# Kernel optimization log

Measured on AMD Instinct MI355X. Metric: run time of the kernel, lower is better.

The kernel has to match this reference:

```python
import jax, jax.numpy as jnp
import numpy as np

NUM_CHANS = 64
LAG = 5
HIDDEN = [32, 32]  # module appends a final 1-channel layer
BATCH = 16
T = 2048


def setup_inputs() -> dict:
    key = jax.random.key(0)
    ks = jax.random.split(key, 7)
    p, h0, h1 = NUM_CHANS, HIDDEN[0], HIDDEN[1]
    # Per-network weights stacked along leading axis n = num_series = p.
    # Xavier-ish scale for layer 0 (Conv1d(p, h0, lag)), default-ish for rest.
    s0 = float(np.sqrt(2.0 / (p * LAG + h0)))
    return {
        "X": jax.random.normal(ks[0], (BATCH, T, p), dtype=jnp.float32),
        "W0": jax.random.normal(ks[1], (p, h0, p, LAG), dtype=jnp.float32) * s0,
        "b0": jax.random.normal(ks[2], (p, h0), dtype=jnp.float32) * 0.01,
        "W1": jax.random.normal(ks[3], (p, h1, h0), dtype=jnp.float32) * float(np.sqrt(1.0 / h0)),
        "b1": jax.random.normal(ks[4], (p, h1), dtype=jnp.float32) * 0.01,
        "W2": jax.random.normal(ks[5], (p, 1, h1), dtype=jnp.float32) * float(np.sqrt(1.0 / h1)),
        "b2": jax.random.normal(ks[6], (p, 1), dtype=jnp.float32) * 0.01,
    }


def reference(X, W0, b0, W1, b1, W2, b2):
    # X: [B, T, p]. Each of n=p networks: Conv1d(p,h0,lag) -> ReLU -> Conv1d(h0,h1,1)
    # -> ReLU -> Conv1d(h1,1,1); outputs concatenated along last dim.
    lag = W0.shape[-1]
    Tout = X.shape[1] - lag + 1  # valid conv output length
    # Sliding windows: Xwin[b,t,c,l] = X[b, t+l, c]  -> [B, Tout, p, lag]
    Xwin = jnp.stack([X[:, l:l + Tout, :] for l in range(lag)], axis=-1)
    # Layer 0 across all n networks at once: [B, n, Tout, h0]
    h = jnp.einsum('btcl,nhcl->bnth', Xwin, W0) + b0[None, :, None, :]
    # 1x1 conv layers (per-network dense along channel dim)
    h = jax.nn.relu(h)
    h = jnp.einsum('bnti,noi->bnto', h, W1) + b1[None, :, None, :]
    h = jax.nn.relu(h)
    h = jnp.einsum('bnti,noi->bnto', h, W2) + b2[None, :, None, :]  # [B, n, Tout, 1]
    # concat along dim 2 of (batch, Tout, 1) per network -> (B, Tout, n)
    return jnp.transpose(h[..., 0], (0, 2, 1))
```

## Files before the change

kernel.cpp:

```cpp
#include <hip/hip_runtime.h>

#define NCH 64
#define LAG 5
#define H0 32
#define H1 32
#define TIN 2048
#define TOUT 2044
#define NBATCH 16

#define XSTRIDE 72

typedef __attribute__((ext_vector_type(8))) short short8;
typedef __attribute__((ext_vector_type(4))) short short4v;
typedef __attribute__((ext_vector_type(4))) float f32x4;

__device__ __forceinline__ unsigned short f2bf(float f) {
    unsigned u = __float_as_uint(f);
    u += 0x7fffu + ((u >> 16) & 1u);
    return (unsigned short)(u >> 16);
}

__device__ __forceinline__ unsigned pack2bf_relu(float a, float b) {
    unsigned ua = __float_as_uint(fmaxf(a, 0.0f)) + 0x8000u;
    unsigned ub = __float_as_uint(fmaxf(b, 0.0f)) + 0x8000u;
    return __builtin_amdgcn_perm(ub, ua, 0x07060302u);
}

__device__ __forceinline__ short4v pack4bf_relu(const f32x4& v) {
    union { short4v s; unsigned u[2]; } cv;
    cv.u[0] = pack2bf_relu(v[0], v[1]);
    cv.u[1] = pack2bf_relu(v[2], v[3]);
    return cv.s;
}

__global__ __launch_bounds__(256) void prep_all(
    const float* __restrict__ X,  unsigned short* __restrict__ Xpad,
    const float* __restrict__ W0, unsigned short* __restrict__ W0b,
    const float* __restrict__ W1, unsigned short* __restrict__ W1b,
    const float* __restrict__ W2, unsigned short* __restrict__ W2b)
{
    const int bx = blockIdx.x;
    if (bx < 512) {
        int id  = bx * 256 + threadIdx.x;
        int row = id >> 2, s4 = id & 3;
        const float4* src = (const float4*)(X + (size_t)id * 16);
        unsigned long long v[4];
        #pragma unroll
        for (int k = 0; k < 4; ++k) {
            float4 x = src[k];
            v[k] = (unsigned long long)f2bf(x.x)
                 | ((unsigned long long)f2bf(x.y) << 16)
                 | ((unsigned long long)f2bf(x.z) << 32)
                 | ((unsigned long long)f2bf(x.w) << 48);
        }
        unsigned long long* dst = (unsigned long long*)(Xpad + (size_t)row * XSTRIDE + s4 * 16);
        dst[0] = v[0]; dst[1] = v[1]; dst[2] = v[2]; dst[3] = v[3];
    } else if (bx < 1024) {
        int j = (bx - 512) * 256 + threadIdx.x;
        int nh = j >> 6, c = j & 63;
        const float* src = W0 + (size_t)j * LAG;
        unsigned short* dst = W0b + nh * 320 + c;
        #pragma unroll
        for (int l = 0; l < LAG; ++l) dst[l * 64] = f2bf(src[l]);
    } else if (bx < 1056) {
        int i = ((bx - 1024) * 256 + threadIdx.x) * 8;
        float4 a = *(const float4*)(W1 + i);
        float4 b = *(const float4*)(W1 + i + 4);
        unsigned long long v0 = (unsigned long long)f2bf(a.x)
                              | ((unsigned long long)f2bf(a.y) << 16)
                              | ((unsigned long long)f2bf(a.z) << 32)
                              | ((unsigned long long)f2bf(a.w) << 48);
        unsigned long long v1 = (unsigned long long)f2bf(b.x)
                              | ((unsigned long long)f2bf(b.y) << 16)
                              | ((unsigned long long)f2bf(b.z) << 32)
                              | ((unsigned long long)f2bf(b.w) << 48);
        *(unsigned long long*)(W1b + i)     = v0;
        *(unsigned long long*)(W1b + i + 4) = v1;
    } else {
        int i = threadIdx.x * 8;
        float4 a = *(const float4*)(W2 + i);
        float4 b = *(const float4*)(W2 + i + 4);
        unsigned long long v0 = (unsigned long long)f2bf(a.x)
                              | ((unsigned long long)f2bf(a.y) << 16)
                              | ((unsigned long long)f2bf(a.z) << 32)
                              | ((unsigned long long)f2bf(a.w) << 48);
        unsigned long long v1 = (unsigned long long)f2bf(b.x)
                              | ((unsigned long long)f2bf(b.y) << 16)
                              | ((unsigned long long)f2bf(b.z) << 32)
                              | ((unsigned long long)f2bf(b.w) << 48);
        *(unsigned long long*)(W2b + i)     = v0;
        *(unsigned long long*)(W2b + i + 4) = v1;
    }
}

__global__ __launch_bounds__(256, 3) void mlp_mfma(
    const unsigned short* __restrict__ Xpad,
    const unsigned short* __restrict__ W0b,
    const unsigned short* __restrict__ W1b,
    const unsigned short* __restrict__ W2b,
    const float* __restrict__ b0, const float* __restrict__ b1,
    const float* __restrict__ b2, float* __restrict__ out)
{
    __shared__ __align__(16) unsigned short xs[37 * 512];
    __shared__ __align__(8)  unsigned short yt[256][4];
    __shared__ __align__(16) float bl[256];
    __shared__ __align__(8)  unsigned at[256 * 10];

    const int tileid = blockIdx.x;
    const int ng     = blockIdx.y;
    const int b      = tileid >> 3;
    const int t0     = (tileid & 7) * 256;
    const int tid    = threadIdx.x;
    const int wave   = tid >> 6;
    const int lane   = tid & 63;
    const int quad   = lane >> 4;
    const int l15    = lane & 15;

    {
        const char* srcb = (const char*)(Xpad + (size_t)(b * TIN + t0) * XSTRIDE);
        #pragma unroll 1
        for (int i = wave; i < 37; i += 4) {
            __builtin_amdgcn_global_load_lds(
                (const __attribute__((address_space(1))) unsigned int*)(srcb + i * 1024 + lane * 16),
                (__attribute__((address_space(3))) unsigned int*)((char*)xs + i * 1024),
                16, 0, 0);
        }
    }

    if (tid < 128)       bl[tid]       = b0[ng * 128 + tid];
    else                 bl[tid]       = b1[ng * 128 + (tid - 128)];

    const int n = ng * 4 + wave;
    short8 B0[10][2];
    const unsigned short* wp0 = W0b + (n * H0 + l15) * (NCH * LAG) + quad * 8;
    #pragma unroll
    for (int ks = 0; ks < 10; ++ks) {
        B0[ks][0] = *(const short8*)(wp0 + ks * 32);
        B0[ks][1] = *(const short8*)(wp0 + 16 * (NCH * LAG) + ks * 32);
    }
    {
        char* rec = (char*)at + tid * 40;
        #pragma unroll
        for (int of = 0; of < 2; ++of)
            #pragma unroll
            for (int kf = 0; kf < 2; ++kf) {
                short4v f = *(const short4v*)(W1b + (n * H1 + of * 16 + l15) * H0 + kf * 16 + quad * 4);
                *(short4v*)(rec + (of * 2 + kf) * 8) = f;
            }
    }
    short4v A2[2];
    #pragma unroll
    for (int kf = 0; kf < 2; ++kf)
        A2[kf] = *(const short4v*)(W2b + n * H1 + kf * 16 + quad * 4);
    const float b2s = __uint_as_float(__builtin_amdgcn_readfirstlane(__float_as_uint(b2[n])));

    __syncthreads();

    const float* bp = bl + wave * 32 + quad * 4;
    const char*  ap = (const char*)at + tid * 40;

    #pragma unroll 1
    for (int chunk = 0; chunk < 8; ++chunk) {
        unsigned loff = 0;
        asm volatile("" : "+v"(loff));

        const int rbase = chunk * 32 + l15;
        const int rowoff0 = rbase * XSTRIDE + quad * 8;
        const int rowoff1 = rowoff0 + 16 * XSTRIDE;

        f32x4 b0v[2], b1v[2];
        b0v[0] = *(const f32x4*)(bp + loff);
        b0v[1] = *(const f32x4*)(bp + loff + 16);
        b1v[0] = *(const f32x4*)(bp + loff + 128);
        b1v[1] = *(const f32x4*)(bp + loff + 144);

        f32x4 acc[2][2];
        acc[0][0] = b0v[0]; acc[0][1] = b0v[1];
        acc[1][0] = b0v[0]; acc[1][1] = b0v[1];
        __builtin_amdgcn_s_setprio(1);
        #pragma unroll
        for (int ks = 0; ks < 10; ++ks) {
            const int xoff = (ks >> 1) * XSTRIDE + (ks & 1) * 32;
            short8 Xf0 = *(const short8*)&xs[rowoff0 + xoff];
            short8 Xf1 = *(const short8*)&xs[rowoff1 + xoff];
            acc[0][0] = __builtin_amdgcn_mfma_f32_16x16x32_bf16(B0[ks][0], Xf0, acc[0][0], 0, 0, 0);
            acc[0][1] = __builtin_amdgcn_mfma_f32_16x16x32_bf16(B0[ks][1], Xf0, acc[0][1], 0, 0, 0);
            acc[1][0] = __builtin_amdgcn_mfma_f32_16x16x32_bf16(B0[ks][0], Xf1, acc[1][0], 0, 0, 0);
            acc[1][1] = __builtin_amdgcn_mfma_f32_16x16x32_bf16(B0[ks][1], Xf1, acc[1][1], 0, 0, 0);
        }
        __builtin_amdgcn_s_setprio(0);

        short4v A1r[4];
        A1r[0] = *(const short4v*)(ap + loff);
        A1r[1] = *(const short4v*)(ap + loff + 8);
        A1r[2] = *(const short4v*)(ap + loff + 16);
        A1r[3] = *(const short4v*)(ap + loff + 24);

        #pragma unroll
        for (int mf = 0; mf < 2; ++mf) {
            short4v Bh0 = pack4bf_relu(acc[mf][0]);
            short4v Bh1 = pack4bf_relu(acc[mf][1]);

            f32x4 D1[2] = { b1v[0], b1v[1] };
            D1[0] = __builtin_amdgcn_mfma_f32_16x16x16bf16_1k(A1r[0], Bh0, D1[0], 0, 0, 0);
            D1[0] = __builtin_amdgcn_mfma_f32_16x16x16bf16_1k(A1r[1], Bh1, D1[0], 0, 0, 0);
            D1[1] = __builtin_amdgcn_mfma_f32_16x16x16bf16_1k(A1r[2], Bh0, D1[1], 0, 0, 0);
            D1[1] = __builtin_amdgcn_mfma_f32_16x16x16bf16_1k(A1r[3], Bh1, D1[1], 0, 0, 0);

            short4v Bg0 = pack4bf_relu(D1[0]);
            short4v Bg1 = pack4bf_relu(D1[1]);

            f32x4 D2 = (f32x4){ b2s, b2s, b2s, b2s };
            D2 = __builtin_amdgcn_mfma_f32_16x16x16bf16_1k(A2[0], Bg0, D2, 0, 0, 0);
            D2 = __builtin_amdgcn_mfma_f32_16x16x16bf16_1k(A2[1], Bg1, D2, 0, 0, 0);

            if (quad == 0)
                yt[chunk * 32 + mf * 16 + l15][wave] = f2bf(D2[0]);
        }
    }
    __syncthreads();

    int t = t0 + tid;
    if (t < TOUT) {
        ushort4 v = *(const ushort4*)yt[tid];
        float4 o;
        o.x = __uint_as_float((unsigned)v.x << 16);
        o.y = __uint_as_float((unsigned)v.y << 16);
        o.z = __uint_as_float((unsigned)v.z << 16);
        o.w = __uint_as_float((unsigned)v.w << 16);
        *(float4*)&out[((size_t)(b * TOUT + t)) * NCH + ng * 4] = o;
    }
}

extern "C" void kernel_launch(void* const* d_in, const int* in_sizes, int n_in,
                              void* d_out, int out_size, void* d_ws, size_t ws_size,
                              hipStream_t stream)
{
    const float* X  = (const float*)d_in[0];
    const float* W0 = (const float*)d_in[1];
    const float* b0 = (const float*)d_in[2];
    const float* W1 = (const float*)d_in[3];
    const float* b1 = (const float*)d_in[4];
    const float* W2 = (const float*)d_in[5];
    const float* b2 = (const float*)d_in[6];
    float* out = (float*)d_out;

    unsigned short* Xpad = (unsigned short*)d_ws;
    unsigned short* W0b  = (unsigned short*)((char*)d_ws + 4726784);
    unsigned short* W1b  = (unsigned short*)((char*)d_ws + 6037504);
    unsigned short* W2b  = (unsigned short*)((char*)d_ws + 6168576);

    prep_all<<<1057, 256, 0, stream>>>(X, Xpad, W0, W0b, W1, W1b, W2, W2b);
    mlp_mfma<<<dim3(128, 16), 256, 0, stream>>>(Xpad, W0b, W1b, W2b, b0, b1, b2, out);
}
```

Measured before the change: 119.3 us.

## Split layer-0 reduction across wave pairs with LDS partial-sum exchange

Each network is now handled by two waves that each compute half of the layer-0 K reduction. The partial accumulators are exchanged through shared memory so each wave finishes layers 1-2 for half the rows. Blocks cover two networks instead of four and the grid doubles, with weights and biases loaded straight into registers. This halves per-wave weight registers and spreads work over more waves, at the cost of per-chunk block barriers, extra LDS traffic and reloading the X tile for twice as many blocks.

```diff
diff --git a/kernel.cpp b/kernel.cpp
--- a/kernel.cpp
+++ b/kernel.cpp
@@ -102,9 +102,9 @@
     const float* __restrict__ b2, float* __restrict__ out)
 {
     __shared__ __align__(16) unsigned short xs[37 * 512];
-    __shared__ __align__(8)  unsigned short yt[256][4];
-    __shared__ __align__(16) float bl[256];
-    __shared__ __align__(8)  unsigned at[256 * 10];
+    __shared__ __align__(16) f32x4 exA[4][64];
+    __shared__ __align__(16) f32x4 exB[4][64];
+    __shared__ __align__(8)  unsigned short yt[256][2];
 
     const int tileid = blockIdx.x;
     const int ng     = blockIdx.y;
@@ -115,6 +115,8 @@
     const int lane   = tid & 63;
     const int quad   = lane >> 4;
     const int l15    = lane & 15;
+    const int nl     = wave >> 1;
+    const int kh     = wave & 1;
 
     {
         const char* srcb = (const char*)(Xpad + (size_t)(b * TIN + t0) * XSTRIDE);
@@ -127,108 +129,97 @@
         }
     }
 
-    if (tid < 128)       bl[tid]       = b0[ng * 128 + tid];
-    else                 bl[tid]       = b1[ng * 128 + (tid - 128)];
-
-    const int n = ng * 4 + wave;
-    short8 B0[10][2];
-    const unsigned short* wp0 = W0b + (n * H0 + l15) * (NCH * LAG) + quad * 8;
-    #pragma unroll
-    for (int ks = 0; ks < 10; ++ks) {
-        B0[ks][0] = *(const short8*)(wp0 + ks * 32);
-        B0[ks][1] = *(const short8*)(wp0 + 16 * (NCH * LAG) + ks * 32);
-    }
-    {
-        char* rec = (char*)at + tid * 40;
-        #pragma unroll
-        for (int of = 0; of < 2; ++of)
-            #pragma unroll
-            for (int kf = 0; kf < 2; ++kf) {
-                short4v f = *(const short4v*)(W1b + (n * H1 + of * 16 + l15) * H0 + kf * 16 + quad * 4);
-                *(short4v*)(rec + (of * 2 + kf) * 8) = f;
-            }
-    }
+    const int n = ng * 2 + nl;
+    short8 B0h[5][2];
+    const unsigned short* wp0 = W0b + (n * H0 + l15) * (NCH * LAG) + quad * 8 + kh * 160;
+    #pragma unroll
+    for (int j = 0; j < 5; ++j) {
+        B0h[j][0] = *(const short8*)(wp0 + j * 32);
+        B0h[j][1] = *(const short8*)(wp0 + 16 * (NCH * LAG) + j * 32);
+    }
+    short4v A1[2][2];
+    #pragma unroll
+    for (int of = 0; of < 2; ++of)
+        #pragma unroll
+        for (int kf = 0; kf < 2; ++kf)
+            A1[of][kf] = *(const short4v*)(W1b + (n * H1 + of * 16 + l15) * H0 + kf * 16 + quad * 4);
     short4v A2[2];
     #pragma unroll
     for (int kf = 0; kf < 2; ++kf)
         A2[kf] = *(const short4v*)(W2b + n * H1 + kf * 16 + quad * 4);
+    f32x4 b0q[2], b1q[2];
+    #pragma unroll
+    for (int f = 0; f < 2; ++f) b0q[f] = *(const f32x4*)(b0 + (size_t)n * H0 + f * 16 + quad * 4);
+    #pragma unroll
+    for (int f = 0; f < 2; ++f) b1q[f] = *(const f32x4*)(b1 + (size_t)n * H1 + f * 16 + quad * 4);
     const float b2s = __uint_as_float(__builtin_amdgcn_readfirstlane(__float_as_uint(b2[n])));
 
+    const int kh5 = kh * 5;
+
     __syncthreads();
-
-    const float* bp = bl + wave * 32 + quad * 4;
-    const char*  ap = (const char*)at + tid * 40;
 
     #pragma unroll 1
     for (int chunk = 0; chunk < 8; ++chunk) {
-        unsigned loff = 0;
-        asm volatile("" : "+v"(loff));
-
-        const int rbase = chunk * 32 + l15;
-        const int rowoff0 = rbase * XSTRIDE + quad * 8;
+        const int rowoff0 = (chunk * 32 + l15) * XSTRIDE + quad * 8;
         const int rowoff1 = rowoff0 + 16 * XSTRIDE;
 
-        f32x4 b0v[2], b1v[2];
-        b0v[0] = *(const f32x4*)(bp + loff);
-        b0v[1] = *(const f32x4*)(bp + loff + 16);
-        b1v[0] = *(const f32x4*)(bp + loff + 128);
-        b1v[1] = *(const f32x4*)(bp + loff + 144);
-
-        f32x4 acc[2][2];
-        acc[0][0] = b0v[0]; acc[0][1] = b0v[1];
-        acc[1][0] = b0v[0]; acc[1][1] = b0v[1];
+        f32x4 p00, p01, p10, p11;
+        if (kh == 0) { p00 = b0q[0]; p01 = b0q[1]; p10 = b0q[0]; p11 = b0q[1]; }
+        else {
+            f32x4 z = (f32x4){0.f, 0.f, 0.f, 0.f};
+            p00 = z; p01 = z; p10 = z; p11 = z;
+        }
         __builtin_amdgcn_s_setprio(1);
         #pragma unroll
-        for (int ks = 0; ks < 10; ++ks) {
+        for (int j = 0; j < 5; ++j) {
+            const int ks   = kh5 + j;
             const int xoff = (ks >> 1) * XSTRIDE + (ks & 1) * 32;
             short8 Xf0 = *(const short8*)&xs[rowoff0 + xoff];
             short8 Xf1 = *(const short8*)&xs[rowoff1 + xoff];
-            acc[0][0] = __builtin_amdgcn_mfma_f32_16x16x32_bf16(B0[ks][0], Xf0, acc[0][0], 0, 0, 0);
-            acc[0][1] = __builtin_amdgcn_mfma_f32_16x16x32_bf16(B0[ks][1], Xf0, acc[0][1], 0, 0, 0);
-            acc[1][0] = __builtin_amdgcn_mfma_f32_16x16x32_bf16(B0[ks][0], Xf1, acc[1][0], 0, 0, 0);
-            acc[1][1] = __builtin_amdgcn_mfma_f32_16x16x32_bf16(B0[ks][1], Xf1, acc[1][1], 0, 0, 0);
+            p00 = __builtin_amdgcn_mfma_f32_16x16x32_bf16(B0h[j][0], Xf0, p00, 0, 0, 0);
+            p01 = __builtin_amdgcn_mfma_f32_16x16x32_bf16(B0h[j][1], Xf0, p01, 0, 0, 0);
+            p10 = __builtin_amdgcn_mfma_f32_16x16x32_bf16(B0h[j][0], Xf1, p10, 0, 0, 0);
+            p11 = __builtin_amdgcn_mfma_f32_16x16x32_bf16(B0h[j][1], Xf1, p11, 0, 0, 0);
         }
         __builtin_amdgcn_s_setprio(0);
 
-        short4v A1r[4];
-        A1r[0] = *(const short4v*)(ap + loff);
-        A1r[1] = *(const short4v*)(ap + loff + 8);
-        A1r[2] = *(const short4v*)(ap + loff + 16);
-        A1r[3] = *(const short4v*)(ap + loff + 24);
-
-        #pragma unroll
-        for (int mf = 0; mf < 2; ++mf) {
-            short4v Bh0 = pack4bf_relu(acc[mf][0]);
-            short4v Bh1 = pack4bf_relu(acc[mf][1]);
-
-            f32x4 D1[2] = { b1v[0], b1v[1] };
-            D1[0] = __builtin_amdgcn_mfma_f32_16x16x16bf16_1k(A1r[0], Bh0, D1[0], 0, 0, 0);
-            D1[0] = __builtin_amdgcn_mfma_f32_16x16x16bf16_1k(A1r[1], Bh1, D1[0], 0, 0, 0);
-            D1[1] = __builtin_amdgcn_mfma_f32_16x16x16bf16_1k(A1r[2], Bh0, D1[1], 0, 0, 0);
-            D1[1] = __builtin_amdgcn_mfma_f32_16x16x16bf16_1k(A1r[3], Bh1, D1[1], 0, 0, 0);
-
-            short4v Bg0 = pack4bf_relu(D1[0]);
-            short4v Bg1 = pack4bf_relu(D1[1]);
-
-            f32x4 D2 = (f32x4){ b2s, b2s, b2s, b2s };
-            D2 = __builtin_amdgcn_mfma_f32_16x16x16bf16_1k(A2[0], Bg0, D2, 0, 0, 0);
-            D2 = __builtin_amdgcn_mfma_f32_16x16x16bf16_1k(A2[1], Bg1, D2, 0, 0, 0);
-
-            if (quad == 0)
-                yt[chunk * 32 + mf * 16 + l15][wave] = f2bf(D2[0]);
-        }
-    }
-    __syncthreads();
+        if (kh == 0) { exA[wave][lane] = p10; exB[wave][lane] = p11; }
+        else         { exA[wave][lane] = p00; exB[wave][lane] = p01; }
+        __syncthreads();
+        f32x4 rA = exA[wave ^ 1][lane];
+        f32x4 rB = exB[wave ^ 1][lane];
+        f32x4 fA = (kh == 0 ? p00 : p10) + rA;
+        f32x4 fB = (kh == 0 ? p01 : p11) + rB;
+
+        short4v Bh0 = pack4bf_relu(fA);
+        short4v Bh1 = pack4bf_relu(fB);
+
+        f32x4 D1[2] = { b1q[0], b1q[1] };
+        D1[0] = __builtin_amdgcn_mfma_f32_16x16x16bf16_1k(A1[0][0], Bh0, D1[0], 0, 0, 0);
+        D1[0] = __builtin_amdgcn_mfma_f32_16x16x16bf16_1k(A1[0][1], Bh1, D1[0], 0, 0, 0);
+        D1[1] = __builtin_amdgcn_mfma_f32_16x16x16bf16_1k(A1[1][0], Bh0, D1[1], 0, 0, 0);
+        D1[1] = __builtin_amdgcn_mfma_f32_16x16x16bf16_1k(A1[1][1], Bh1, D1[1], 0, 0, 0);
+
+        short4v Bg0 = pack4bf_relu(D1[0]);
+        short4v Bg1 = pack4bf_relu(D1[1]);
+
+        f32x4 D2 = (f32x4){ b2s, b2s, b2s, b2s };
+        D2 = __builtin_amdgcn_mfma_f32_16x16x16bf16_1k(A2[0], Bg0, D2, 0, 0, 0);
+        D2 = __builtin_amdgcn_mfma_f32_16x16x16bf16_1k(A2[1], Bg1, D2, 0, 0, 0);
+
+        if (quad == 0)
+            yt[chunk * 32 + kh * 16 + l15][nl] = f2bf(D2[0]);
+
+        __syncthreads();
+    }
 
     int t = t0 + tid;
     if (t < TOUT) {
-        ushort4 v = *(const ushort4*)yt[tid];
-        float4 o;
-        o.x = __uint_as_float((unsigned)v.x << 16);
-        o.y = __uint_as_float((unsigned)v.y << 16);
-        o.z = __uint_as_float((unsigned)v.z << 16);
-        o.w = __uint_as_float((unsigned)v.w << 16);
-        *(float4*)&out[((size_t)(b * TOUT + t)) * NCH + ng * 4] = o;
+        unsigned v = *(const unsigned*)yt[tid];
+        float2 o;
+        o.x = __uint_as_float((v & 0xffffu) << 16);
+        o.y = __uint_as_float(v & 0xffff0000u);
+        *(float2*)&out[((size_t)(b * TOUT + t)) * NCH + ng * 2] = o;
     }
 }
 
@@ -251,5 +242,5 @@
     unsigned short* W2b  = (unsigned short*)((char*)d_ws + 6168576);
 
     prep_all<<<1057, 256, 0, stream>>>(X, Xpad, W0, W0b, W1, W1b, W2, W2b);
-    mlp_mfma<<<dim3(128, 16), 256, 0, stream>>>(Xpad, W0b, W1b, W2b, b0, b1, b2, out);
-}
+    mlp_mfma<<<dim3(128, 32), 256, 0, stream>>>(Xpad, W0b, W1b, W2b, b0, b1, b2, out);
+}
```

New measurement: 129.9 us. 8.9% more time.
